# Optimization experiments

Hardware: AMD Instinct MI355X
Metric: run time of the kernel (lower is better)

The kernel has to match this reference:

```python
import jax, jax.numpy as jnp
import numpy as np


def setup_inputs() -> dict:
    key = jax.random.key(0)
    ks = jax.random.split(key, 7)
    B, T, I, H, O = 256, 512, 64, 512, 24
    s_ih = 1.0 / np.sqrt(H)
    return {
        "x":    jax.random.normal(ks[0], (B, T, I), dtype=jnp.float32),
        "W_ih": jax.random.normal(ks[1], (H, I), dtype=jnp.float32) * s_ih,
        "W_hh": jax.random.normal(ks[2], (H, H), dtype=jnp.float32) * s_ih,
        "b_ih": jax.random.normal(ks[3], (H,), dtype=jnp.float32) * s_ih,
        "b_hh": jax.random.normal(ks[4], (H,), dtype=jnp.float32) * s_ih,
        "fc_w": jax.random.normal(ks[5], (O, H), dtype=jnp.float32) * s_ih,
        "fc_b": jax.random.normal(ks[6], (O,), dtype=jnp.float32) * s_ih,
    }


def reference(x, W_ih, W_hh, b_ih, b_hh, fc_w, fc_b):
    # PyTorch nn.RNN(nonlinearity='relu', batch_first=True):
    #   h_t = relu(x_t @ W_ih^T + b_ih + h_{t-1} @ W_hh^T + b_hh), h_0 = 0
    B, T, I = x.shape
    H = W_hh.shape[0]
    # Precompute input projections for all timesteps in one GEMM: [B, T, H]
    xw = jnp.einsum('bti,hi->bth', x, W_ih) + (b_ih + b_hh)

    def step(h, xw_t):
        h = jax.nn.relu(xw_t + h @ W_hh.T)  # [B, H]
        return h, None

    h0 = jnp.zeros((B, H), dtype=x.dtype)
    h_last, _ = jax.lax.scan(step, h0, jnp.swapaxes(xw, 0, 1))  # scan over T
    # Final linear on last timestep's hidden state: [B, O]
    return h_last @ fc_w.T + fc_b
```

## Files before the change

### kernel.cpp

```cpp
#include <hip/hip_runtime.h>


#define T_STEPS 512
#define NG      16
#define NM      8
#define SLAB    32768
#define FLAGS_OFF (2 * NG * SLAB)
#define NEG_OFF  (FLAGS_OFF + NG * 64)
#define POLL_CAP 100000
#define TAG_CAP  20000
#define NEG_CAP  20000000

#define LA_STRIDE 1040
#define LA_PLANE  16640
#define LA_PAR    33280
#define LX_OFF    66560
#define LX_STRIDE 144
#define LX_PLANE  2304

typedef short          short8  __attribute__((ext_vector_type(8)));
typedef unsigned short bfx4    __attribute__((ext_vector_type(4)));
typedef unsigned       uintx4  __attribute__((ext_vector_type(4)));
typedef float          floatx4 __attribute__((ext_vector_type(4)));
typedef unsigned long long ull;

__device__ __forceinline__ unsigned short f2bf(float x) {
    unsigned u = __float_as_uint(x);
    u = (u + 0x7fffu + ((u >> 16) & 1u)) >> 16;
    return (unsigned short)u;
}
__device__ __forceinline__ float bf2f(unsigned short h) {
    return __uint_as_float(((unsigned)h) << 16);
}
__device__ __forceinline__ void st_ag_u32(void* p, unsigned v) {
    __hip_atomic_store((unsigned*)p, v, __ATOMIC_RELAXED, __HIP_MEMORY_SCOPE_AGENT);
}
__device__ __forceinline__ unsigned ld_ag_u32(const void* p) {
    return __hip_atomic_load((const unsigned*)p, __ATOMIC_RELAXED, __HIP_MEMORY_SCOPE_AGENT);
}
__device__ __forceinline__ uintx4 ld_l3_b128_async(const void* p) {
    uintx4 v;
    asm volatile("global_load_dwordx4 %0, %1, off sc0 sc1"
                 : "=v"(v) : "v"(p) : "memory");
    return v;
}
__device__ __forceinline__ void st_l3_b32(void* p, unsigned v) {
    asm volatile("global_store_dword %0, %1, off sc0 sc1"
                 :: "v"(p), "v"(v) : "memory");
}
__device__ __forceinline__ void st_l3_b128(void* p, uintx4 v) {
    asm volatile("global_store_dwordx4 %0, %1, off sc0 sc1"
                 :: "v"(p), "v"(v) : "memory");
}
__device__ __forceinline__ void wait_vm0() {
    asm volatile("s_waitcnt vmcnt(0)" ::: "memory");
}
__device__ __forceinline__ void poll_flag(const unsigned* p, unsigned want) {
    int it = 0;
    for (;;) {
        unsigned f = ld_ag_u32(p);
        if (f == want || f == want + 1u) return;
        if (++it >= POLL_CAP) return;
    }
}

__global__ __launch_bounds__(256, 1) void rnn_persistent(
    const float* __restrict__ x,     const float* __restrict__ W_ih,
    const float* __restrict__ W_hh,  const float* __restrict__ b_ih,
    const float* __restrict__ b_hh,  const float* __restrict__ fc_w,
    const float* __restrict__ fc_b,  float* __restrict__ out,
    unsigned char* __restrict__ ws)
{
    const int tid  = threadIdx.x;
    const int lane = tid & 63;
    const int w    = tid >> 6;
    const int n    = lane & 15;
    const int quad = lane >> 4;

    const int bid = blockIdx.x;
    const int g = bid >> 3;
    const int m = bid & 7;

    unsigned char* ex = (unsigned char*)ws;
    unsigned* flagbase = (unsigned*)(ex + FLAGS_OFF + g * 64);
    __shared__ __align__(16) unsigned char smem[LX_OFF + 2 * LX_PLANE];
    __shared__ unsigned sh_nonce;

    unsigned* nonce_p = (unsigned*)(ex + NEG_OFF);
    if (tid == 0) {
        if (bid == 0) {
            unsigned nn = ((unsigned)__builtin_amdgcn_s_memrealtime() << 8) | 0x5Bu;
            st_ag_u32(nonce_p, nn);
        }
        unsigned v; int it = 0;
        do { v = ld_ag_u32(nonce_p); } while ((v & 0xFFu) != 0x5Bu && ++it < NEG_CAP);
        sh_nonce = v;
    }
    __syncthreads();
    const unsigned nonce = sh_nonce;

    const int wrow = m * 64 + w * 16 + n;
    short8 Whi[18], Wlo[18];
    #pragma unroll
    for (int kt = 0; kt < 18; ++kt) {
        const float* p = (kt < 16) ? (W_hh + wrow * 512 + kt * 32 + quad * 8)
                                   : (W_ih + wrow * 64 + (kt - 16) * 32 + quad * 8);
        #pragma unroll
        for (int jj = 0; jj < 8; ++jj) {
            float f = p[jj];
            unsigned short h = f2bf(f);
            Whi[kt][jj] = (short)h;
            Wlo[kt][jj] = (short)f2bf(f - bf2f(h));
        }
    }
    const float bias_i = b_ih[wrow] + b_hh[wrow];

    const int prow = tid >> 4, pc4 = tid & 15;
    int poff[7];
    #pragma unroll
    for (int r = 0; r < 7; ++r) {
        const int pm = r + (r >= m ? 1 : 0);
        poff[r] = prow * 2048 + pm * 256 + pc4 * 16;
    }

    {
        uintx4 z = {0u, 0u, 0u, 0u};
        st_l3_b128(ex + g * SLAB + prow * 2048 + m * 256 + pc4 * 16, z);
        #pragma unroll
        for (int r = 0; r < 4; ++r) {
            const int row = quad * 4 + r;
            *(unsigned short*)(smem + 0 * LA_PLANE + row * LA_STRIDE + wrow * 2) = 0;
            *(unsigned short*)(smem + LA_PLANE + row * LA_STRIDE + wrow * 2) = 0;
        }
    }
    wait_vm0();
    __syncthreads();
    if (tid == 0) st_ag_u32(flagbase + m, nonce);

    const int xrow = tid >> 4, xi4 = tid & 15;
    for (int t = 0; t < T_STEPS; ++t) {
        const unsigned texp = (((unsigned)t >> 1) & 1u) << 31;
        const unsigned char* slab_r = ex + ((t & 1) * NG + g) * SLAB;

        uintx4 P[7];
        #pragma unroll
        for (int r = 0; r < 7; ++r) P[r] = ld_l3_b128_async(slab_r + poff[r]);
        const float4 xv = *(const float4*)
            (x + ((size_t)(g * 16 + xrow) * T_STEPS + t) * 64 + xi4 * 4);

        if (tid < 7) {
            const int pm = tid + (tid >= m ? 1 : 0);
            poll_flag(flagbase + pm, nonce + (unsigned)t);
        }
        wait_vm0();
        __syncthreads();

        {
            int it = 0;
            for (;;) {
                unsigned bad = 0;
                #pragma unroll
                for (int r = 0; r < 7; ++r)
                    bad |= (P[r].x ^ texp) | (P[r].y ^ texp)
                         | (P[r].z ^ texp) | (P[r].w ^ texp);
                if (!(bad & 0x80000000u) || ++it >= TAG_CAP) break;
                #pragma unroll
                for (int r = 0; r < 7; ++r) P[r] = ld_l3_b128_async(slab_r + poff[r]);
                wait_vm0();
            }
        }

        unsigned char* abase = smem + (t & 1) * LA_PAR;
        #pragma unroll
        for (int r = 0; r < 7; ++r) {
            const int pm = r + (r >= m ? 1 : 0);
            ull hi = 0, lo = 0;
            #pragma unroll
            for (int j = 0; j < 4; ++j) {
                const float f = __uint_as_float(P[r][j] & 0x7fffffffu);
                const unsigned short hs = f2bf(f);
                const unsigned short ls = f2bf(f - bf2f(hs));
                hi |= (ull)hs << (16 * j);
                lo |= (ull)ls << (16 * j);
            }
            const int base = prow * LA_STRIDE + pm * 128 + pc4 * 8;
            *(ull*)(abase + base)            = hi;
            *(ull*)(abase + LA_PLANE + base) = lo;
        }
        {
            ull hi = 0, lo = 0;
            #pragma unroll
            for (int k = 0; k < 4; ++k) {
                const float f = (k == 0) ? xv.x : (k == 1) ? xv.y : (k == 2) ? xv.z : xv.w;
                const unsigned short hs = f2bf(f);
                const unsigned short ls = f2bf(f - bf2f(hs));
                hi |= (ull)hs << (16 * k);
                lo |= (ull)ls << (16 * k);
            }
            *(ull*)(smem + LX_OFF + xrow * LX_STRIDE + xi4 * 8)            = hi;
            *(ull*)(smem + LX_OFF + LX_PLANE + xrow * LX_STRIDE + xi4 * 8) = lo;
        }
        __syncthreads();

        floatx4 c0 = {0.f,0.f,0.f,0.f}, c1 = {0.f,0.f,0.f,0.f}, c2 = {0.f,0.f,0.f,0.f};
        #pragma unroll
        for (int kt = 0; kt < 16; ++kt) {
            const unsigned char* ba = abase + n * LA_STRIDE + kt * 64 + quad * 16;
            short8 ah = *(const short8*)(ba);
            short8 al = *(const short8*)(ba + LA_PLANE);
            c0 = __builtin_amdgcn_mfma_f32_16x16x32_bf16(ah, Whi[kt], c0, 0, 0, 0);
            c1 = __builtin_amdgcn_mfma_f32_16x16x32_bf16(al, Whi[kt], c1, 0, 0, 0);
            c2 = __builtin_amdgcn_mfma_f32_16x16x32_bf16(ah, Wlo[kt], c2, 0, 0, 0);
        }
        #pragma unroll
        for (int kt = 16; kt < 18; ++kt) {
            const unsigned char* ba = smem + LX_OFF + n * LX_STRIDE + (kt - 16) * 64 + quad * 16;
            short8 ah = *(const short8*)(ba);
            short8 al = *(const short8*)(ba + LX_PLANE);
            c0 = __builtin_amdgcn_mfma_f32_16x16x32_bf16(ah, Whi[kt], c0, 0, 0, 0);
            c1 = __builtin_amdgcn_mfma_f32_16x16x32_bf16(al, Whi[kt], c1, 0, 0, 0);
            c2 = __builtin_amdgcn_mfma_f32_16x16x32_bf16(ah, Wlo[kt], c2, 0, 0, 0);
        }

        const unsigned otag = ((((unsigned)t + 1u) >> 1) & 1u) << 31;
        unsigned char* slab_w = ex + (((t + 1) & 1) * NG + g) * SLAB;
        unsigned char* obase  = smem + ((t + 1) & 1) * LA_PAR;
        const floatx4 cs = c0 + c1 + c2;
        #pragma unroll
        for (int r = 0; r < 4; ++r) {
            float v = cs[r] + bias_i;
            v = v > 0.f ? v : 0.f;
            const int row = quad * 4 + r;
            const unsigned short h = f2bf(v);
            const unsigned short l = f2bf(v - bf2f(h));
            *(unsigned short*)(obase + row * LA_STRIDE + wrow * 2) = h;
            *(unsigned short*)(obase + LA_PLANE + row * LA_STRIDE + wrow * 2) = l;
            st_l3_b32(slab_w + row * 2048 + wrow * 4, __float_as_uint(v) | otag);
        }
        if (tid == 0) st_ag_u32(flagbase + m, nonce + (unsigned)t + 1u);
    }

    if (m != 0) return;
    {
        const unsigned texp = 0;
        const unsigned char* slab_r = ex + (0 * NG + g) * SLAB;
        uintx4 P[7];
        #pragma unroll
        for (int r = 0; r < 7; ++r) P[r] = ld_l3_b128_async(slab_r + poff[r]);
        if (tid < 7) poll_flag(flagbase + (tid + 1), nonce + (unsigned)T_STEPS);
        wait_vm0();
        __syncthreads();
        int it = 0;
        for (;;) {
            unsigned bad = 0;
            #pragma unroll
            for (int r = 0; r < 7; ++r)
                bad |= (P[r].x ^ texp) | (P[r].y ^ texp)
                     | (P[r].z ^ texp) | (P[r].w ^ texp);
            if (!(bad & 0x80000000u) || ++it >= TAG_CAP) break;
            #pragma unroll
            for (int r = 0; r < 7; ++r) P[r] = ld_l3_b128_async(slab_r + poff[r]);
            wait_vm0();
        }
        unsigned char* abase = smem;
        #pragma unroll
        for (int r = 0; r < 7; ++r) {
            const int pm = r + 1;
            ull hi = 0, lo = 0;
            #pragma unroll
            for (int j = 0; j < 4; ++j) {
                const float f = __uint_as_float(P[r][j] & 0x7fffffffu);
                const unsigned short hs = f2bf(f);
                const unsigned short ls = f2bf(f - bf2f(hs));
                hi |= (ull)hs << (16 * j);
                lo |= (ull)ls << (16 * j);
            }
            const int base = prow * LA_STRIDE + pm * 128 + pc4 * 8;
            *(ull*)(abase + base)            = hi;
            *(ull*)(abase + LA_PLANE + base) = lo;
        }
    }
    __syncthreads();
    for (int idx = tid; idx < 384; idx += 256) {
        const int row = idx / 24, o = idx % 24;
        const float* wp = fc_w + o * 512;
        float s = 0.f;
        for (int k = 0; k < 512; k += 4) {
            bfx4 hv = *(const bfx4*)(smem + row * LA_STRIDE + k * 2);
            bfx4 lv = *(const bfx4*)(smem + LA_PLANE + row * LA_STRIDE + k * 2);
            const float4 wv = *(const float4*)(wp + k);
            s += (bf2f(hv[0]) + bf2f(lv[0])) * wv.x;
            s += (bf2f(hv[1]) + bf2f(lv[1])) * wv.y;
            s += (bf2f(hv[2]) + bf2f(lv[2])) * wv.z;
            s += (bf2f(hv[3]) + bf2f(lv[3])) * wv.w;
        }
        out[(g * 16 + row) * 24 + o] = s + fc_b[o];
    }
}

extern "C" void kernel_launch(void* const* d_in, const int* in_sizes, int n_in,
                              void* d_out, int out_size, void* d_ws, size_t ws_size,
                              hipStream_t stream) {
    (void)in_sizes; (void)n_in; (void)out_size; (void)ws_size;
    const float* x    = (const float*)d_in[0];
    const float* W_ih = (const float*)d_in[1];
    const float* W_hh = (const float*)d_in[2];
    const float* b_ih = (const float*)d_in[3];
    const float* b_hh = (const float*)d_in[4];
    const float* fc_w = (const float*)d_in[5];
    const float* fc_b = (const float*)d_in[6];
    rnn_persistent<<<128, 256, 0, stream>>>(x, W_ih, W_hh, b_ih, b_hh,
                                            fc_w, fc_b, (float*)d_out,
                                            (unsigned char*)d_ws);
}
```

Before: 1.642 ms.

## Halve blocks per batch group and use packed bf16 conversion

Each batch group is now split across 4 cooperating blocks instead of 8. Each wave computes two 16-row output tiles with doubled register-resident weights, so every timestep has fewer peer flags to poll and fewer cross-block slab exchanges. The scalar bf16 hi/lo split is replaced by the packed v_cvt_pk_bf16_f32 instruction. In exchange the grid drops to 64 blocks, so fewer CUs are used and each block does twice the MFMA work per step. Weight register pressure also doubles, which risks spills.

```diff
diff --git a/kernel.cpp b/kernel.cpp
--- a/kernel.cpp
+++ b/kernel.cpp
@@ -3,7 +3,7 @@
 
 #define T_STEPS 512
 #define NG      16
-#define NM      8
+#define NM      4
 #define SLAB    32768
 #define FLAGS_OFF (2 * NG * SLAB)
 #define NEG_OFF  (FLAGS_OFF + NG * 64)
@@ -31,6 +31,22 @@
 }
 __device__ __forceinline__ float bf2f(unsigned short h) {
     return __uint_as_float(((unsigned)h) << 16);
+}
+__device__ __forceinline__ unsigned cvtpk(float a, float b) {
+    unsigned r;
+    asm("v_cvt_pk_bf16_f32 %0, %1, %2" : "=v"(r) : "v"(a), "v"(b));
+    return r;
+}
+__device__ __forceinline__ void pack_hilo(float f0, float f1, float f2, float f3,
+                                          ull& hi, ull& lo) {
+    const unsigned h01 = cvtpk(f0, f1), h23 = cvtpk(f2, f3);
+    const float l0 = f0 - __uint_as_float(h01 << 16);
+    const float l1 = f1 - __uint_as_float(h01 & 0xffff0000u);
+    const float l2 = f2 - __uint_as_float(h23 << 16);
+    const float l3 = f3 - __uint_as_float(h23 & 0xffff0000u);
+    const unsigned q01 = cvtpk(l0, l1), q23 = cvtpk(l2, l3);
+    hi = (ull)h01 | ((ull)h23 << 32);
+    lo = (ull)q01 | ((ull)q23 << 32);
 }
 __device__ __forceinline__ void st_ag_u32(void* p, unsigned v) {
     __hip_atomic_store((unsigned*)p, v, __ATOMIC_RELAXED, __HIP_MEMORY_SCOPE_AGENT);
@@ -78,8 +94,8 @@
     const int quad = lane >> 4;
 
     const int bid = blockIdx.x;
-    const int g = bid >> 3;
-    const int m = bid & 7;
+    const int g = bid >> 2;
+    const int m = bid & 3;
 
     unsigned char* ex = (unsigned char*)ws;
     unsigned* flagbase = (unsigned*)(ex + FLAGS_OFF + g * 64);
@@ -99,38 +115,50 @@
     __syncthreads();
     const unsigned nonce = sh_nonce;
 
-    const int wrow = m * 64 + w * 16 + n;
-    short8 Whi[18], Wlo[18];
+    const int wrow0 = m * 128 + w * 32 + n;
+    const int wrow1 = wrow0 + 16;
+    short8 Whi0[18], Wlo0[18], Whi1[18], Wlo1[18];
     #pragma unroll
     for (int kt = 0; kt < 18; ++kt) {
-        const float* p = (kt < 16) ? (W_hh + wrow * 512 + kt * 32 + quad * 8)
-                                   : (W_ih + wrow * 64 + (kt - 16) * 32 + quad * 8);
+        const float* p0 = (kt < 16) ? (W_hh + wrow0 * 512 + kt * 32 + quad * 8)
+                                    : (W_ih + wrow0 * 64 + (kt - 16) * 32 + quad * 8);
+        const float* p1 = (kt < 16) ? (W_hh + wrow1 * 512 + kt * 32 + quad * 8)
+                                    : (W_ih + wrow1 * 64 + (kt - 16) * 32 + quad * 8);
         #pragma unroll
         for (int jj = 0; jj < 8; ++jj) {
-            float f = p[jj];
-            unsigned short h = f2bf(f);
-            Whi[kt][jj] = (short)h;
-            Wlo[kt][jj] = (short)f2bf(f - bf2f(h));
-        }
-    }
-    const float bias_i = b_ih[wrow] + b_hh[wrow];
+            float f0 = p0[jj];
+            unsigned short h0 = f2bf(f0);
+            Whi0[kt][jj] = (short)h0;
+            Wlo0[kt][jj] = (short)f2bf(f0 - bf2f(h0));
+            float f1 = p1[jj];
+            unsigned short h1 = f2bf(f1);
+            Whi1[kt][jj] = (short)h1;
+            Wlo1[kt][jj] = (short)f2bf(f1 - bf2f(h1));
+        }
+    }
+    const float bias0 = b_ih[wrow0] + b_hh[wrow0];
+    const float bias1 = b_ih[wrow1] + b_hh[wrow1];
 
     const int prow = tid >> 4, pc4 = tid & 15;
-    int poff[7];
+    int poff[6];
     #pragma unroll
-    for (int r = 0; r < 7; ++r) {
+    for (int r = 0; r < 3; ++r) {
         const int pm = r + (r >= m ? 1 : 0);
-        poff[r] = prow * 2048 + pm * 256 + pc4 * 16;
+        poff[2 * r]     = prow * 2048 + pm * 512 + pc4 * 16;
+        poff[2 * r + 1] = prow * 2048 + pm * 512 + 256 + pc4 * 16;
     }
 
     {
         uintx4 z = {0u, 0u, 0u, 0u};
-        st_l3_b128(ex + g * SLAB + prow * 2048 + m * 256 + pc4 * 16, z);
+        st_l3_b128(ex + g * SLAB + prow * 2048 + m * 512 + pc4 * 16, z);
+        st_l3_b128(ex + g * SLAB + prow * 2048 + m * 512 + 256 + pc4 * 16, z);
         #pragma unroll
         for (int r = 0; r < 4; ++r) {
             const int row = quad * 4 + r;
-            *(unsigned short*)(smem + 0 * LA_PLANE + row * LA_STRIDE + wrow * 2) = 0;
-            *(unsigned short*)(smem + LA_PLANE + row * LA_STRIDE + wrow * 2) = 0;
+            *(unsigned short*)(smem + row * LA_STRIDE + wrow0 * 2) = 0;
+            *(unsigned short*)(smem + LA_PLANE + row * LA_STRIDE + wrow0 * 2) = 0;
+            *(unsigned short*)(smem + row * LA_STRIDE + wrow1 * 2) = 0;
+            *(unsigned short*)(smem + LA_PLANE + row * LA_STRIDE + wrow1 * 2) = 0;
         }
     }
     wait_vm0();
@@ -142,13 +170,13 @@
         const unsigned texp = (((unsigned)t >> 1) & 1u) << 31;
         const unsigned char* slab_r = ex + ((t & 1) * NG + g) * SLAB;
 
-        uintx4 P[7];
-        #pragma unroll
-        for (int r = 0; r < 7; ++r) P[r] = ld_l3_b128_async(slab_r + poff[r]);
+        uintx4 P[6];
+        #pragma unroll
+        for (int r = 0; r < 6; ++r) P[r] = ld_l3_b128_async(slab_r + poff[r]);
         const float4 xv = *(const float4*)
             (x + ((size_t)(g * 16 + xrow) * T_STEPS + t) * 64 + xi4 * 4);
 
-        if (tid < 7) {
+        if (tid < 3) {
             const int pm = tid + (tid >= m ? 1 : 0);
             poll_flag(flagbase + pm, nonce + (unsigned)t);
         }
@@ -160,82 +188,119 @@
             for (;;) {
                 unsigned bad = 0;
                 #pragma unroll
-                for (int r = 0; r < 7; ++r)
+                for (int r = 0; r < 6; ++r)
                     bad |= (P[r].x ^ texp) | (P[r].y ^ texp)
                          | (P[r].z ^ texp) | (P[r].w ^ texp);
                 if (!(bad & 0x80000000u) || ++it >= TAG_CAP) break;
                 #pragma unroll
-                for (int r = 0; r < 7; ++r) P[r] = ld_l3_b128_async(slab_r + poff[r]);
+                for (int r = 0; r < 6; ++r) P[r] = ld_l3_b128_async(slab_r + poff[r]);
                 wait_vm0();
             }
         }
 
         unsigned char* abase = smem + (t & 1) * LA_PAR;
         #pragma unroll
-        for (int r = 0; r < 7; ++r) {
-            const int pm = r + (r >= m ? 1 : 0);
-            ull hi = 0, lo = 0;
-            #pragma unroll
-            for (int j = 0; j < 4; ++j) {
-                const float f = __uint_as_float(P[r][j] & 0x7fffffffu);
-                const unsigned short hs = f2bf(f);
-                const unsigned short ls = f2bf(f - bf2f(hs));
-                hi |= (ull)hs << (16 * j);
-                lo |= (ull)ls << (16 * j);
-            }
-            const int base = prow * LA_STRIDE + pm * 128 + pc4 * 8;
+        for (int r = 0; r < 6; ++r) {
+            const int pp = r >> 1;
+            const int pm = pp + (pp >= m ? 1 : 0);
+            const int half = r & 1;
+            ull hi, lo;
+            pack_hilo(__uint_as_float(P[r].x & 0x7fffffffu),
+                      __uint_as_float(P[r].y & 0x7fffffffu),
+                      __uint_as_float(P[r].z & 0x7fffffffu),
+                      __uint_as_float(P[r].w & 0x7fffffffu), hi, lo);
+            const int base = prow * LA_STRIDE + pm * 256 + half * 128 + pc4 * 8;
             *(ull*)(abase + base)            = hi;
             *(ull*)(abase + LA_PLANE + base) = lo;
         }
         {
-            ull hi = 0, lo = 0;
-            #pragma unroll
-            for (int k = 0; k < 4; ++k) {
-                const float f = (k == 0) ? xv.x : (k == 1) ? xv.y : (k == 2) ? xv.z : xv.w;
-                const unsigned short hs = f2bf(f);
-                const unsigned short ls = f2bf(f - bf2f(hs));
-                hi |= (ull)hs << (16 * k);
-                lo |= (ull)ls << (16 * k);
-            }
+            ull hi, lo;
+            pack_hilo(xv.x, xv.y, xv.z, xv.w, hi, lo);
             *(ull*)(smem + LX_OFF + xrow * LX_STRIDE + xi4 * 8)            = hi;
             *(ull*)(smem + LX_OFF + LX_PLANE + xrow * LX_STRIDE + xi4 * 8) = lo;
         }
         __syncthreads();
 
-        floatx4 c0 = {0.f,0.f,0.f,0.f}, c1 = {0.f,0.f,0.f,0.f}, c2 = {0.f,0.f,0.f,0.f};
+        floatx4 c00 = {0.f,0.f,0.f,0.f}, c01 = {0.f,0.f,0.f,0.f}, c02 = {0.f,0.f,0.f,0.f};
+        floatx4 c10 = {0.f,0.f,0.f,0.f}, c11 = {0.f,0.f,0.f,0.f}, c12 = {0.f,0.f,0.f,0.f};
         #pragma unroll
         for (int kt = 0; kt < 16; ++kt) {
             const unsigned char* ba = abase + n * LA_STRIDE + kt * 64 + quad * 16;
             short8 ah = *(const short8*)(ba);
             short8 al = *(const short8*)(ba + LA_PLANE);
-            c0 = __builtin_amdgcn_mfma_f32_16x16x32_bf16(ah, Whi[kt], c0, 0, 0, 0);
-            c1 = __builtin_amdgcn_mfma_f32_16x16x32_bf16(al, Whi[kt], c1, 0, 0, 0);
-            c2 = __builtin_amdgcn_mfma_f32_16x16x32_bf16(ah, Wlo[kt], c2, 0, 0, 0);
+            c00 = __builtin_amdgcn_mfma_f32_16x16x32_bf16(ah, Whi0[kt], c00, 0, 0, 0);
+            c01 = __builtin_amdgcn_mfma_f32_16x16x32_bf16(al, Whi0[kt], c01, 0, 0, 0);
+            c02 = __builtin_amdgcn_mfma_f32_16x16x32_bf16(ah, Wlo0[kt], c02, 0, 0, 0);
+            c10 = __builtin_amdgcn_mfma_f32_16x16x32_bf16(ah, Whi1[kt], c10, 0, 0, 0);
+            c11 = __builtin_amdgcn_mfma_f32_16x16x32_bf16(al, Whi1[kt], c11, 0, 0, 0);
+            c12 = __builtin_amdgcn_mfma_f32_16x16x32_bf16(ah, Wlo1[kt], c12, 0, 0, 0);
         }
         #pragma unroll
         for (int kt = 16; kt < 18; ++kt) {
             const unsigned char* ba = smem + LX_OFF + n * LX_STRIDE + (kt - 16) * 64 + quad * 16;
             short8 ah = *(const short8*)(ba);
             short8 al = *(const short8*)(ba + LX_PLANE);
-            c0 = __builtin_amdgcn_mfma_f32_16x16x32_bf16(ah, Whi[kt], c0, 0, 0, 0);
-            c1 = __builtin_amdgcn_mfma_f32_16x16x32_bf16(al, Whi[kt], c1, 0, 0, 0);
-            c2 = __builtin_amdgcn_mfma_f32_16x16x32_bf16(ah, Wlo[kt], c2, 0, 0, 0);
+            c00 = __builtin_amdgcn_mfma_f32_16x16x32_bf16(ah, Whi0[kt], c00, 0, 0, 0);
+            c01 = __builtin_amdgcn_mfma_f32_16x16x32_bf16(al, Whi0[kt], c01, 0, 0, 0);
+            c02 = __builtin_amdgcn_mfma_f32_16x16x32_bf16(ah, Wlo0[kt], c02, 0, 0, 0);
+            c10 = __builtin_amdgcn_mfma_f32_16x16x32_bf16(ah, Whi1[kt], c10, 0, 0, 0);
+            c11 = __builtin_amdgcn_mfma_f32_16x16x32_bf16(al, Whi1[kt], c11, 0, 0, 0);
+            c12 = __builtin_amdgcn_mfma_f32_16x16x32_bf16(ah, Wlo1[kt], c12, 0, 0, 0);
         }
 
         const unsigned otag = ((((unsigned)t + 1u) >> 1) & 1u) << 31;
         unsigned char* slab_w = ex + (((t + 1) & 1) * NG + g) * SLAB;
         unsigned char* obase  = smem + ((t + 1) & 1) * LA_PAR;
-        const floatx4 cs = c0 + c1 + c2;
-        #pragma unroll
-        for (int r = 0; r < 4; ++r) {
-            float v = cs[r] + bias_i;
-            v = v > 0.f ? v : 0.f;
-            const int row = quad * 4 + r;
-            const unsigned short h = f2bf(v);
-            const unsigned short l = f2bf(v - bf2f(h));
-            *(unsigned short*)(obase + row * LA_STRIDE + wrow * 2) = h;
-            *(unsigned short*)(obase + LA_PLANE + row * LA_STRIDE + wrow * 2) = l;
-            st_l3_b32(slab_w + row * 2048 + wrow * 4, __float_as_uint(v) | otag);
+        const int r0 = quad * 4;
+        {
+            const floatx4 cs = c00 + c01 + c02;
+            const float v0 = fmaxf(cs[0] + bias0, 0.f);
+            const float v1 = fmaxf(cs[1] + bias0, 0.f);
+            const float v2 = fmaxf(cs[2] + bias0, 0.f);
+            const float v3 = fmaxf(cs[3] + bias0, 0.f);
+            const unsigned h01 = cvtpk(v0, v1), h23 = cvtpk(v2, v3);
+            const float l0 = v0 - __uint_as_float(h01 << 16);
+            const float l1 = v1 - __uint_as_float(h01 & 0xffff0000u);
+            const float l2 = v2 - __uint_as_float(h23 << 16);
+            const float l3 = v3 - __uint_as_float(h23 & 0xffff0000u);
+            const unsigned q01 = cvtpk(l0, l1), q23 = cvtpk(l2, l3);
+            *(unsigned short*)(obase + (r0+0) * LA_STRIDE + wrow0 * 2) = (unsigned short)(h01 & 0xffffu);
+            *(unsigned short*)(obase + (r0+1) * LA_STRIDE + wrow0 * 2) = (unsigned short)(h01 >> 16);
+            *(unsigned short*)(obase + (r0+2) * LA_STRIDE + wrow0 * 2) = (unsigned short)(h23 & 0xffffu);
+            *(unsigned short*)(obase + (r0+3) * LA_STRIDE + wrow0 * 2) = (unsigned short)(h23 >> 16);
+            *(unsigned short*)(obase + LA_PLANE + (r0+0) * LA_STRIDE + wrow0 * 2) = (unsigned short)(q01 & 0xffffu);
+            *(unsigned short*)(obase + LA_PLANE + (r0+1) * LA_STRIDE + wrow0 * 2) = (unsigned short)(q01 >> 16);
+            *(unsigned short*)(obase + LA_PLANE + (r0+2) * LA_STRIDE + wrow0 * 2) = (unsigned short)(q23 & 0xffffu);
+            *(unsigned short*)(obase + LA_PLANE + (r0+3) * LA_STRIDE + wrow0 * 2) = (unsigned short)(q23 >> 16);
+            st_l3_b32(slab_w + (r0+0) * 2048 + wrow0 * 4, __float_as_uint(v0) | otag);
+            st_l3_b32(slab_w + (r0+1) * 2048 + wrow0 * 4, __float_as_uint(v1) | otag);
+            st_l3_b32(slab_w + (r0+2) * 2048 + wrow0 * 4, __float_as_uint(v2) | otag);
+            st_l3_b32(slab_w + (r0+3) * 2048 + wrow0 * 4, __float_as_uint(v3) | otag);
+        }
+        {
+            const floatx4 cs = c10 + c11 + c12;
+            const float v0 = fmaxf(cs[0] + bias1, 0.f);
+            const float v1 = fmaxf(cs[1] + bias1, 0.f);
+            const float v2 = fmaxf(cs[2] + bias1, 0.f);
+            const float v3 = fmaxf(cs[3] + bias1, 0.f);
+            const unsigned h01 = cvtpk(v0, v1), h23 = cvtpk(v2, v3);
+            const float l0 = v0 - __uint_as_float(h01 << 16);
+            const float l1 = v1 - __uint_as_float(h01 & 0xffff0000u);
+            const float l2 = v2 - __uint_as_float(h23 << 16);
+            const float l3 = v3 - __uint_as_float(h23 & 0xffff0000u);
+            const unsigned q01 = cvtpk(l0, l1), q23 = cvtpk(l2, l3);
+            *(unsigned short*)(obase + (r0+0) * LA_STRIDE + wrow1 * 2) = (unsigned short)(h01 & 0xffffu);
+            *(unsigned short*)(obase + (r0+1) * LA_STRIDE + wrow1 * 2) = (unsigned short)(h01 >> 16);
+            *(unsigned short*)(obase + (r0+2) * LA_STRIDE + wrow1 * 2) = (unsigned short)(h23 & 0xffffu);
+            *(unsigned short*)(obase + (r0+3) * LA_STRIDE + wrow1 * 2) = (unsigned short)(h23 >> 16);
+            *(unsigned short*)(obase + LA_PLANE + (r0+0) * LA_STRIDE + wrow1 * 2) = (unsigned short)(q01 & 0xffffu);
+            *(unsigned short*)(obase + LA_PLANE + (r0+1) * LA_STRIDE + wrow1 * 2) = (unsigned short)(q01 >> 16);
+            *(unsigned short*)(obase + LA_PLANE + (r0+2) * LA_STRIDE + wrow1 * 2) = (unsigned short)(q23 & 0xffffu);
+            *(unsigned short*)(obase + LA_PLANE + (r0+3) * LA_STRIDE + wrow1 * 2) = (unsigned short)(q23 >> 16);
+            st_l3_b32(slab_w + (r0+0) * 2048 + wrow1 * 4, __float_as_uint(v0) | otag);
+            st_l3_b32(slab_w + (r0+1) * 2048 + wrow1 * 4, __float_as_uint(v1) | otag);
+            st_l3_b32(slab_w + (r0+2) * 2048 + wrow1 * 4, __float_as_uint(v2) | otag);
+            st_l3_b32(slab_w + (r0+3) * 2048 + wrow1 * 4, __float_as_uint(v3) | otag);
         }
         if (tid == 0) st_ag_u32(flagbase + m, nonce + (unsigned)t + 1u);
     }
@@ -244,38 +309,35 @@
     {
         const unsigned texp = 0;
         const unsigned char* slab_r = ex + (0 * NG + g) * SLAB;
-        uintx4 P[7];
-        #pragma unroll
-        for (int r = 0; r < 7; ++r) P[r] = ld_l3_b128_async(slab_r + poff[r]);
-        if (tid < 7) poll_flag(flagbase + (tid + 1), nonce + (unsigned)T_STEPS);
+        uintx4 P[6];
+        #pragma unroll
+        for (int r = 0; r < 6; ++r) P[r] = ld_l3_b128_async(slab_r + poff[r]);
+        if (tid < 3) poll_flag(flagbase + (tid + 1), nonce + (unsigned)T_STEPS);
         wait_vm0();
         __syncthreads();
         int it = 0;
         for (;;) {
             unsigned bad = 0;
             #pragma unroll
-            for (int r = 0; r < 7; ++r)
+            for (int r = 0; r < 6; ++r)
                 bad |= (P[r].x ^ texp) | (P[r].y ^ texp)
                      | (P[r].z ^ texp) | (P[r].w ^ texp);
             if (!(bad & 0x80000000u) || ++it >= TAG_CAP) break;
             #pragma unroll
-            for (int r = 0; r < 7; ++r) P[r] = ld_l3_b128_async(slab_r + poff[r]);
+            for (int r = 0; r < 6; ++r) P[r] = ld_l3_b128_async(slab_r + poff[r]);
             wait_vm0();
         }
         unsigned char* abase = smem;
         #pragma unroll
-        for (int r = 0; r < 7; ++r) {
-            const int pm = r + 1;
-            ull hi = 0, lo = 0;
-            #pragma unroll
-            for (int j = 0; j < 4; ++j) {
-                const float f = __uint_as_float(P[r][j] & 0x7fffffffu);
-                const unsigned short hs = f2bf(f);
-                const unsigned short ls = f2bf(f - bf2f(hs));
-                hi |= (ull)hs << (16 * j);
-                lo |= (ull)ls << (16 * j);
-            }
-            const int base = prow * LA_STRIDE + pm * 128 + pc4 * 8;
+        for (int r = 0; r < 6; ++r) {
+            const int pm = (r >> 1) + 1;
+            const int half = r & 1;
+            ull hi, lo;
+            pack_hilo(__uint_as_float(P[r].x & 0x7fffffffu),
+                      __uint_as_float(P[r].y & 0x7fffffffu),
+                      __uint_as_float(P[r].z & 0x7fffffffu),
+                      __uint_as_float(P[r].w & 0x7fffffffu), hi, lo);
+            const int base = prow * LA_STRIDE + pm * 256 + half * 128 + pc4 * 8;
             *(ull*)(abase + base)            = hi;
             *(ull*)(abase + LA_PLANE + base) = lo;
         }
@@ -309,7 +371,7 @@
     const float* b_hh = (const float*)d_in[4];
     const float* fc_w = (const float*)d_in[5];
     const float* fc_b = (const float*)d_in[6];
-    rnn_persistent<<<128, 256, 0, stream>>>(x, W_ih, W_hh, b_ih, b_hh,
-                                            fc_w, fc_b, (float*)d_out,
-                                            (unsigned char*)d_ws);
-}
+    rnn_persistent<<<NG * NM, 256, 0, stream>>>(x, W_ih, W_hh, b_ih, b_hh,
+                                                fc_w, fc_b, (float*)d_out,
+                                                (unsigned char*)d_ws);
+}
```

Result: slower. 1.940 ms (+18.2%).
